# Optimization experiments

Measured on AMD Instinct MI355X. Metric: run time of the kernel, lower is better.

The kernel has to match this reference:

```python
import jax, jax.numpy as jnp
import numpy as np

IN_LEN = 65536
OUT_CH = 512
KERNEL = 32
STRIDE = 16
PAD = 8
FOLD = (IN_LEN + 2 * PAD - KERNEL) // STRIDE + 1  # 4096
BATCH = 64


def setup_inputs() -> dict:
    key = jax.random.key(0)
    kx, kw = jax.random.split(key)
    x = jax.random.normal(kx, (BATCH, IN_LEN), dtype=jnp.float32)
    # learned per-position weights: [fold_num, kernel_size, out_channels]
    weight = jax.random.normal(kw, (FOLD, KERNEL, OUT_CH), dtype=jnp.float32)
    return {"x": x, "weight": weight}


def reference(x, weight):
    # pad last dim with zeros on both sides
    xp = jnp.pad(x, ((0, 0), (PAD, PAD)))  # [B, L + 2*PAD]
    # unfold: gather overlapping windows [B, FOLD, KERNEL]
    idx = jnp.arange(FOLD)[:, None] * STRIDE + jnp.arange(KERNEL)[None, :]  # [FOLD, KERNEL]
    windows = xp[:, idx]  # [B, FOLD, KERNEL]
    out = jnp.einsum("bfk,fko->bfo", windows, weight)  # [B, FOLD, OUT_CH]
    return out
```

## Files before the change

kernel.cpp:

```cpp
#include <hip/hip_runtime.h>

constexpr int B       = 64;
constexpr int F       = 4096;
constexpr int K       = 32;
constexpr int O       = 512;
constexpr int STRIDE  = 16;
constexpr int PAD     = 8;
constexpr int IN_LEN  = 65536;

constexpr int O_TILE  = 256;
constexpr int BLOCK   = 256;

__global__ __launch_bounds__(BLOCK)
void Local_39152921870765_kernel(const float* __restrict__ x,
                                 const float* __restrict__ w,
                                 float* __restrict__ out)
{
    const int f   = blockIdx.y;
    const int o0  = blockIdx.x * O_TILE;
    const int tid = threadIdx.x;

    __shared__ float w_s[K][O_TILE];
    __shared__ float x_s[K][B];

    {
        const float4* wg  = (const float4*)(w + (size_t)f * K * O + o0);
        float4*       ws4 = (float4*)(&w_s[0][0]);
        #pragma unroll
        for (int j = tid; j < (K * O_TILE) / 4; j += BLOCK) {
            const int k  = j >> 6;
            const int o4 = j & 63;
            ws4[j] = wg[k * (O / 4) + o4];
        }
    }

    {
        const int b    = tid >> 2;
        const int kq   = (tid & 3) * 8;
        const int base = f * STRIDE - PAD;
        #pragma unroll
        for (int i = 0; i < 8; ++i) {
            const int k  = kq + i;
            const int gi = base + k;
            float v = 0.0f;
            if (gi >= 0 && gi < IN_LEN) v = x[(size_t)b * IN_LEN + gi];
            x_s[k][b] = v;
        }
    }
    __syncthreads();

    const int og = tid & 31;
    const int bg = tid >> 5;
    const int ob = og * 4;
    const int bb = bg * 8;

    float acc[8][8];
    #pragma unroll
    for (int i = 0; i < 8; ++i)
        #pragma unroll
        for (int j = 0; j < 8; ++j) acc[i][j] = 0.0f;

    #pragma unroll 4
    for (int k = 0; k < K; ++k) {
        const float4 w0 = *(const float4*)&w_s[k][ob];
        const float4 w1 = *(const float4*)&w_s[k][ob + 128];
        const float4 xa = *(const float4*)&x_s[k][bb];
        const float4 xb = *(const float4*)&x_s[k][bb + 4];
        const float xv[8] = {xa.x, xa.y, xa.z, xa.w, xb.x, xb.y, xb.z, xb.w};
        const float wv[8] = {w0.x, w0.y, w0.z, w0.w, w1.x, w1.y, w1.z, w1.w};
        #pragma unroll
        for (int i = 0; i < 8; ++i)
            #pragma unroll
            for (int j = 0; j < 8; ++j)
                acc[i][j] = fmaf(xv[i], wv[j], acc[i][j]);
    }

    #pragma unroll
    for (int i = 0; i < 8; ++i) {
        const size_t base = ((size_t)(bb + i) * F + f) * O + o0;
        const float4 v0 = make_float4(acc[i][0], acc[i][1], acc[i][2], acc[i][3]);
        const float4 v1 = make_float4(acc[i][4], acc[i][5], acc[i][6], acc[i][7]);
        *(float4*)(out + base + ob)       = v0;
        *(float4*)(out + base + ob + 128) = v1;
    }
}

extern "C" void kernel_launch(void* const* d_in, const int* in_sizes, int n_in,
                              void* d_out, int out_size, void* d_ws, size_t ws_size,
                              hipStream_t stream) {
    const float* x = (const float*)d_in[0];
    const float* w = (const float*)d_in[1];
    float* out = (float*)d_out;

    dim3 grid(O / O_TILE, F);
    Local_39152921870765_kernel<<<grid, BLOCK, 0, stream>>>(x, w, out);
}
```

Baseline: 750.3 us.

## Double-buffer weights via global_load_lds and process multiple fold positions per block

Each block now handles 8 consecutive fold positions across all 512 output channels with 512 threads. The next position's weight slice is staged asynchronously into a second LDS buffer with global_load_lds, and the next x window is prefetched into registers with float4 loads while the current position computes. This aims to hide global memory latency and cut per-block launch overhead. In exchange the grid shrinks to 512 blocks, LDS use roughly doubles per block, and register pressure rises, which could lower occupancy.

```diff
diff --git a/kernel.cpp b/kernel.cpp
--- a/kernel.cpp
+++ b/kernel.cpp
@@ -8,80 +8,105 @@
 constexpr int PAD     = 8;
 constexpr int IN_LEN  = 65536;
 
-constexpr int O_TILE  = 256;
-constexpr int BLOCK   = 256;
+constexpr int FT      = 8;
+constexpr int BLOCK   = 512;
+constexpr int XROW    = 68;
 
-__global__ __launch_bounds__(BLOCK)
+__global__ __launch_bounds__(BLOCK, 2)
 void Local_39152921870765_kernel(const float* __restrict__ x,
                                  const float* __restrict__ w,
                                  float* __restrict__ out)
 {
-    const int f   = blockIdx.y;
-    const int o0  = blockIdx.x * O_TILE;
-    const int tid = threadIdx.x;
+    __shared__ float w_s[2][K][O];
+    __shared__ float x_s[2][K][XROW];
 
-    __shared__ float w_s[K][O_TILE];
-    __shared__ float x_s[K][B];
+    const int tid  = threadIdx.x;
+    const int lane = tid & 63;
+    const int wid  = tid >> 6;
+    const int f0   = blockIdx.x * FT;
 
-    {
-        const float4* wg  = (const float4*)(w + (size_t)f * K * O + o0);
-        float4*       ws4 = (float4*)(&w_s[0][0]);
-        #pragma unroll
-        for (int j = tid; j < (K * O_TILE) / 4; j += BLOCK) {
-            const int k  = j >> 6;
-            const int o4 = j & 63;
-            ws4[j] = wg[k * (O / 4) + o4];
-        }
-    }
+    const int og = lane;
+    const int bb = wid * 8;
 
-    {
-        const int b    = tid >> 2;
-        const int kq   = (tid & 3) * 8;
-        const int base = f * STRIDE - PAD;
+    const int sb = tid >> 3;
+    const int sq = tid & 7;
+
+    auto stage_w = [&](int f, int buf) {
+        const float* gbase = w + (size_t)f * (K * O);
         #pragma unroll
         for (int i = 0; i < 8; ++i) {
-            const int k  = kq + i;
-            const int gi = base + k;
-            float v = 0.0f;
-            if (gi >= 0 && gi < IN_LEN) v = x[(size_t)b * IN_LEN + gi];
-            x_s[k][b] = v;
+            const int c    = wid * 8 + i;
+            const int k    = c >> 1;
+            const int half = c & 1;
+            const float* g = gbase + k * O + half * 256 + lane * 4;
+            __builtin_amdgcn_global_load_lds(
+                (const __attribute__((address_space(1))) void*)g,
+                (__attribute__((address_space(3))) void*)&w_s[buf][k][half * 256],
+                16, 0, 0);
         }
-    }
+    };
+
+    auto load_x = [&](int f) -> float4 {
+        const int p0 = f * STRIDE - PAD + sq * 4;
+        float4 v = make_float4(0.f, 0.f, 0.f, 0.f);
+        if (p0 >= 0 && p0 <= IN_LEN - 4)
+            v = *(const float4*)(x + (size_t)sb * IN_LEN + p0);
+        return v;
+    };
+    auto put_x = [&](int buf, float4 v) {
+        x_s[buf][sq * 4 + 0][sb] = v.x;
+        x_s[buf][sq * 4 + 1][sb] = v.y;
+        x_s[buf][sq * 4 + 2][sb] = v.z;
+        x_s[buf][sq * 4 + 3][sb] = v.w;
+    };
+
+    stage_w(f0, 0);
+    put_x(0, load_x(f0));
     __syncthreads();
 
-    const int og = tid & 31;
-    const int bg = tid >> 5;
-    const int ob = og * 4;
-    const int bb = bg * 8;
+    int cur = 0;
+    for (int ft = 0; ft < FT; ++ft) {
+        const int f   = f0 + ft;
+        const int nxt = cur ^ 1;
+        const bool more = (ft + 1 < FT);
 
-    float acc[8][8];
-    #pragma unroll
-    for (int i = 0; i < 8; ++i)
-        #pragma unroll
-        for (int j = 0; j < 8; ++j) acc[i][j] = 0.0f;
+        float4 xpre;
+        if (more) {
+            stage_w(f + 1, nxt);
+            xpre = load_x(f + 1);
+        }
 
-    #pragma unroll 4
-    for (int k = 0; k < K; ++k) {
-        const float4 w0 = *(const float4*)&w_s[k][ob];
-        const float4 w1 = *(const float4*)&w_s[k][ob + 128];
-        const float4 xa = *(const float4*)&x_s[k][bb];
-        const float4 xb = *(const float4*)&x_s[k][bb + 4];
-        const float xv[8] = {xa.x, xa.y, xa.z, xa.w, xb.x, xb.y, xb.z, xb.w};
-        const float wv[8] = {w0.x, w0.y, w0.z, w0.w, w1.x, w1.y, w1.z, w1.w};
+        float acc[8][8];
         #pragma unroll
         for (int i = 0; i < 8; ++i)
             #pragma unroll
-            for (int j = 0; j < 8; ++j)
-                acc[i][j] = fmaf(xv[i], wv[j], acc[i][j]);
-    }
+            for (int j = 0; j < 8; ++j) acc[i][j] = 0.0f;
 
-    #pragma unroll
-    for (int i = 0; i < 8; ++i) {
-        const size_t base = ((size_t)(bb + i) * F + f) * O + o0;
-        const float4 v0 = make_float4(acc[i][0], acc[i][1], acc[i][2], acc[i][3]);
-        const float4 v1 = make_float4(acc[i][4], acc[i][5], acc[i][6], acc[i][7]);
-        *(float4*)(out + base + ob)       = v0;
-        *(float4*)(out + base + ob + 128) = v1;
+        #pragma unroll 4
+        for (int k = 0; k < K; ++k) {
+            const float4 wa  = *(const float4*)&w_s[cur][k][og * 4];
+            const float4 wb  = *(const float4*)&w_s[cur][k][og * 4 + 256];
+            const float4 xa  = *(const float4*)&x_s[cur][k][bb];
+            const float4 xb4 = *(const float4*)&x_s[cur][k][bb + 4];
+            const float xv[8] = {xa.x, xa.y, xa.z, xa.w, xb4.x, xb4.y, xb4.z, xb4.w};
+            const float wv[8] = {wa.x, wa.y, wa.z, wa.w, wb.x, wb.y, wb.z, wb.w};
+            #pragma unroll
+            for (int i = 0; i < 8; ++i)
+                #pragma unroll
+                for (int j = 0; j < 8; ++j)
+                    acc[i][j] = fmaf(xv[i], wv[j], acc[i][j]);
+        }
+
+        #pragma unroll
+        for (int i = 0; i < 8; ++i) {
+            const size_t base = ((size_t)(bb + i) * F + f) * O + og * 4;
+            *(float4*)(out + base)       = make_float4(acc[i][0], acc[i][1], acc[i][2], acc[i][3]);
+            *(float4*)(out + base + 256) = make_float4(acc[i][4], acc[i][5], acc[i][6], acc[i][7]);
+        }
+
+        if (more) put_x(nxt, xpre);
+        __syncthreads();
+        cur = nxt;
     }
 }
 
@@ -92,6 +117,6 @@
     const float* w = (const float*)d_in[1];
     float* out = (float*)d_out;
 
-    dim3 grid(O / O_TILE, F);
+    dim3 grid(F / FT);
     Local_39152921870765_kernel<<<grid, BLOCK, 0, stream>>>(x, w, out);
 }
```

After: 730.1 us. -2.7%, faster.
